# Kernel tuning notes

Hardware: AMD Instinct MI355X
Metric: run time of the kernel (lower is better)

Reference implementation:

```python
import jax, jax.numpy as jnp
import numpy as np

N_HEAD = 16
OUTPUT_DIM = 1024
HEAD_DIM = OUTPUT_DIM // N_HEAD  # 64


def setup_inputs() -> dict:
    key = jax.random.key(0)
    kq, kk, kv = jax.random.split(key, 3)
    B, S, D = 4, 2048, OUTPUT_DIM
    return {
        "Q": jax.random.normal(kq, (B, S, D), dtype=jnp.float32),
        "K": jax.random.normal(kk, (B, S, D), dtype=jnp.float32),
        "V": jax.random.normal(kv, (B, S, D), dtype=jnp.float32),
    }


def reference(Q, K, V):
    # FAITHFUL to the original Keras layer: it reshapes Q into K and V as well
    # (K = reshape(Q, ...), V = reshape(Q, ...)), so the K and V inputs are
    # ignored and attention is computed of Q against itself.
    B, S, _ = Q.shape
    q = Q.reshape(B, S, N_HEAD, HEAD_DIM)  # [B,S,H,D]
    scale = 1.0 / np.sqrt(HEAD_DIM).astype(np.float32)
    # scores: [B,H,S,S]
    scores = jnp.einsum("bshd,bthd->bhst", q, q) * scale
    attn = jax.nn.softmax(scores, axis=-1)
    out = jnp.einsum("bhst,bthd->bshd", attn, q)  # [B,S,H,D]
    # concat of per-head slices along last axis == head-major reshape
    return out.reshape(B, S, N_HEAD * HEAD_DIM)
```

## Files before the change

### kernel.cpp

```cpp
#include <hip/hip_runtime.h>
#include <stdint.h>

#define S_LEN 2048
#define DH    64
#define NH    16
#define DM    1024
#define NBH   64

typedef float    f32x4 __attribute__((ext_vector_type(4)));
typedef _Float16 half8 __attribute__((ext_vector_type(8)));
typedef _Float16 half4 __attribute__((ext_vector_type(4)));

#define GL_LDS_B128(g, l) \
  __builtin_amdgcn_global_load_lds((const __attribute__((address_space(1))) void*)(g), \
                                   (__attribute__((address_space(3))) void*)(l), 16, 0, 0)

__global__ __launch_bounds__(256) void preprocess_kernel(const float* __restrict__ Q,
                                                         _Float16* __restrict__ Qh,
                                                         _Float16* __restrict__ QhT) {
    const int t  = threadIdx.x;
    const int st = blockIdx.x & 31;
    const int bh = blockIdx.x >> 5;
    const int b = bh >> 4, h = bh & 15;
    const int s0 = (t & 15) * 4;
    const int d0 = (t >> 4) * 4;
    const float* src = Q + (size_t)b * S_LEN * DM + (size_t)(st * 64) * DM + h * DH;

    half4 hv[4];
    #pragma unroll
    for (int i = 0; i < 4; ++i) {
        const float4 v = *(const float4*)(src + (size_t)(s0 + i) * DM + d0);
        hv[i] = (half4){ (_Float16)v.x, (_Float16)v.y, (_Float16)v.z, (_Float16)v.w };
    }
    _Float16* qh = Qh + ((size_t)bh * S_LEN + st * 64) * DH;
    #pragma unroll
    for (int i = 0; i < 4; ++i)
        *(half4*)(qh + (s0 + i) * DH + d0) = hv[i];
    _Float16* qt = QhT + (size_t)bh * DH * S_LEN + st * 64;
    #pragma unroll
    for (int j = 0; j < 4; ++j) {
        const half4 tv = (half4){ hv[0][j], hv[1][j], hv[2][j], hv[3][j] };
        *(half4*)(qt + (size_t)(d0 + j) * S_LEN + s0) = tv;
    }
}

__global__ __launch_bounds__(128, 2) void attn_v3_kernel(const _Float16* __restrict__ Qh,
                                                         const _Float16* __restrict__ QhT,
                                                         float* __restrict__ out) {
    __shared__ __align__(16) _Float16 KnS[64 * 64];
    __shared__ __align__(16) _Float16 KtS[64 * 64];
    __shared__ __align__(16) _Float16 Pb[2][64 * 64];

    const int tid  = threadIdx.x;
    const int w    = tid >> 6;
    const int lane = tid & 63;
    const int quad = lane >> 4;
    const int l15  = lane & 15;
    const int xq   = l15 & 7;
    const int qblk = blockIdx.x & 15;
    const int bh   = blockIdx.x >> 4;
    const int q0   = qblk * 128 + w * 64;

    const _Float16* qh_bh = Qh + (size_t)bh * S_LEN * DH;
    const _Float16* qt_bh = QhT + (size_t)bh * DH * S_LEN;

    half8 qreg[4][2];
    #pragma unroll
    for (int nch = 0; nch < 4; ++nch) {
        const _Float16* p = qh_bh + (size_t)(q0 + nch * 16 + l15) * DH + quad * 8;
        qreg[nch][0] = *(const half8*)p;
        qreg[nch][1] = *(const half8*)(p + 32);
    }

    const float qs = 0.18033688011112042f;
    float m_c[4];
    #pragma unroll
    for (int nch = 0; nch < 4; ++nch) {
        float part = 0.f;
        #pragma unroll
        for (int s = 0; s < 2; ++s)
            #pragma unroll
            for (int j = 0; j < 8; ++j) { const float x = (float)qreg[nch][s][j]; part += x * x; }
        part += __shfl_xor(part, 16, 64);
        part += __shfl_xor(part, 32, 64);
        m_c[nch] = qs * part;
    }

    const _Float16* kn_src[4]; _Float16* kn_dst[4];
    const _Float16* kt_src[4]; _Float16* kt_dst[4];
    #pragma unroll
    for (int i = 0; i < 4; ++i) {
        const int ch = i * 128 + tid;
        const int row = ch >> 3, c = ch & 7;
        kn_src[i] = qh_bh + row * DH + ((c ^ (row & 7)) * 8);
        kn_dst[i] = &KnS[ch * 8];
        kt_src[i] = qt_bh + (size_t)row * S_LEN + ((c ^ (row & 7)) * 8);
        kt_dst[i] = &KtS[ch * 8];
    }

    f32x4 O[4][4];
    #pragma unroll
    for (int m = 0; m < 4; ++m)
        #pragma unroll
        for (int n = 0; n < 4; ++n) O[m][n] = (f32x4){0.f, 0.f, 0.f, 0.f};
    float lsum[4] = {0.f, 0.f, 0.f, 0.f};
    _Float16* Pw = Pb[w];

    for (int t = 0; t < S_LEN / 64; ++t) {
        __syncthreads();
        #pragma unroll
        for (int i = 0; i < 4; ++i) GL_LDS_B128(kn_src[i] + t * (64 * DH), kn_dst[i]);
        #pragma unroll
        for (int i = 0; i < 4; ++i) GL_LDS_B128(kt_src[i] + t * 64, kt_dst[i]);
        __syncthreads();

        #pragma unroll
        for (int mch = 0; mch < 4; ++mch) {
            const half8 a0 = *(const half8*)&KnS[(mch * 16 + l15) * 64 + ((quad ^ xq) * 8)];
            const half8 a1 = *(const half8*)&KnS[(mch * 16 + l15) * 64 + (((4 + quad) ^ xq) * 8)];
            const int wc   = 2 * mch + (quad >> 1);
            const int woff = (quad & 1) * 4;
            #pragma unroll
            for (int nch = 0; nch < 4; ++nch) {
                f32x4 acc = (f32x4){0.f, 0.f, 0.f, 0.f};
                acc = __builtin_amdgcn_mfma_f32_16x16x32_f16(a0, qreg[nch][0], acc, 0, 0, 0);
                acc = __builtin_amdgcn_mfma_f32_16x16x32_f16(a1, qreg[nch][1], acc, 0, 0, 0);
                const float p0 = __builtin_amdgcn_exp2f(__builtin_fmaf(acc[0], qs, -m_c[nch]));
                const float p1 = __builtin_amdgcn_exp2f(__builtin_fmaf(acc[1], qs, -m_c[nch]));
                const float p2 = __builtin_amdgcn_exp2f(__builtin_fmaf(acc[2], qs, -m_c[nch]));
                const float p3 = __builtin_amdgcn_exp2f(__builtin_fmaf(acc[3], qs, -m_c[nch]));
                lsum[nch] += (p0 + p1) + (p2 + p3);
                const half4 hv = (half4){ (_Float16)p0, (_Float16)p1, (_Float16)p2, (_Float16)p3 };
                *(half4*)&Pw[(nch * 16 + l15) * 64 + ((wc ^ xq) * 8) + woff] = hv;
            }
        }

        half8 pf[4][2];
        #pragma unroll
        for (int mch = 0; mch < 4; ++mch) {
            pf[mch][0] = *(const half8*)&Pw[(mch * 16 + l15) * 64 + ((quad ^ xq) * 8)];
            pf[mch][1] = *(const half8*)&Pw[(mch * 16 + l15) * 64 + (((4 + quad) ^ xq) * 8)];
        }
        #pragma unroll
        for (int nch = 0; nch < 4; ++nch) {
            const half8 v0 = *(const half8*)&KtS[(nch * 16 + l15) * 64 + ((quad ^ xq) * 8)];
            const half8 v1 = *(const half8*)&KtS[(nch * 16 + l15) * 64 + (((4 + quad) ^ xq) * 8)];
            #pragma unroll
            for (int mch = 0; mch < 4; ++mch) {
                O[mch][nch] = __builtin_amdgcn_mfma_f32_16x16x32_f16(pf[mch][0], v0, O[mch][nch], 0, 0, 0);
                O[mch][nch] = __builtin_amdgcn_mfma_f32_16x16x32_f16(pf[mch][1], v1, O[mch][nch], 0, 0, 0);
            }
        }
    }

    float lcol[4];
    #pragma unroll
    for (int nch = 0; nch < 4; ++nch) {
        float l = lsum[nch];
        l += __shfl_xor(l, 16, 64);
        l += __shfl_xor(l, 32, 64);
        lcol[nch] = l;
    }
    const int b = bh >> 4, h = bh & 15;
    float* ob = out + (size_t)b * S_LEN * DM + h * DH;
    #pragma unroll
    for (int mch = 0; mch < 4; ++mch) {
        float inv[4];
        #pragma unroll
        for (int r = 0; r < 4; ++r)
            inv[r] = 1.0f / __shfl(lcol[mch], quad * 4 + r, 16);
        #pragma unroll
        for (int nch = 0; nch < 4; ++nch)
            #pragma unroll
            for (int r = 0; r < 4; ++r)
                ob[(size_t)(q0 + mch * 16 + quad * 4 + r) * DM + nch * 16 + l15] = O[mch][nch][r] * inv[r];
    }
}

extern "C" void kernel_launch(void* const* d_in, const int* in_sizes, int n_in,
                              void* d_out, int out_size, void* d_ws, size_t ws_size,
                              hipStream_t stream) {
    const float* Q = (const float*)d_in[0];
    float* out = (float*)d_out;
    _Float16* Qh  = (_Float16*)d_ws;
    _Float16* QhT = Qh + (size_t)NBH * S_LEN * DH;
    preprocess_kernel<<<dim3(NBH * (S_LEN / 64)), dim3(256), 0, stream>>>(Q, Qh, QhT);
    attn_v3_kernel<<<dim3(NBH * (S_LEN / 128)), dim3(128), 0, stream>>>(Qh, QhT, out);
}
```

Baseline: 215.0 us.

## Split attention blocks into four 32-query waves and transpose via LDS in preprocess

The attention kernel now runs 256 threads per block, with four waves of 32 queries each instead of two waves of 64, and launch bounds allow more blocks per CU. Each wave holds half the accumulator and Q registers, which is meant to raise occupancy and latency hiding. In exchange, each K tile staged in LDS feeds fewer MFMAs per wave, so there is more LDS traffic and barrier overhead per unit of work. The preprocess kernel now stages a 64x64 tile in padded LDS so both the fp16 row-major and transposed outputs are written with coalesced 16-byte stores.

```diff
diff --git a/kernel.cpp b/kernel.cpp
--- a/kernel.cpp
+++ b/kernel.cpp
@@ -18,38 +18,57 @@
 __global__ __launch_bounds__(256) void preprocess_kernel(const float* __restrict__ Q,
                                                          _Float16* __restrict__ Qh,
                                                          _Float16* __restrict__ QhT) {
+    __shared__ __align__(16) _Float16 tile[64][72];
     const int t  = threadIdx.x;
     const int st = blockIdx.x & 31;
     const int bh = blockIdx.x >> 5;
     const int b = bh >> 4, h = bh & 15;
-    const int s0 = (t & 15) * 4;
-    const int d0 = (t >> 4) * 4;
-    const float* src = Q + (size_t)b * S_LEN * DM + (size_t)(st * 64) * DM + h * DH;
-
-    half4 hv[4];
-    #pragma unroll
-    for (int i = 0; i < 4; ++i) {
-        const float4 v = *(const float4*)(src + (size_t)(s0 + i) * DM + d0);
-        hv[i] = (half4){ (_Float16)v.x, (_Float16)v.y, (_Float16)v.z, (_Float16)v.w };
-    }
-    _Float16* qh = Qh + ((size_t)bh * S_LEN + st * 64) * DH;
-    #pragma unroll
-    for (int i = 0; i < 4; ++i)
-        *(half4*)(qh + (s0 + i) * DH + d0) = hv[i];
-    _Float16* qt = QhT + (size_t)bh * DH * S_LEN + st * 64;
-    #pragma unroll
-    for (int j = 0; j < 4; ++j) {
-        const half4 tv = (half4){ hv[0][j], hv[1][j], hv[2][j], hv[3][j] };
-        *(half4*)(qt + (size_t)(d0 + j) * S_LEN + s0) = tv;
+    const int s0 = st * 64;
+
+    {
+        const int r = t >> 2;
+        const int c = (t & 3) * 16;
+        const float* src = Q + ((size_t)b * S_LEN + s0 + r) * DM + h * DH + c;
+        #pragma unroll
+        for (int i = 0; i < 4; ++i) {
+            const float4 v = ((const float4*)src)[i];
+            *(half4*)&tile[r][c + 4 * i] =
+                (half4){ (_Float16)v.x, (_Float16)v.y, (_Float16)v.z, (_Float16)v.w };
+        }
+    }
+    __syncthreads();
+
+    {
+        const int s = t >> 2;
+        const int c = (t & 3) * 16;
+        const half8 a = *(const half8*)&tile[s][c];
+        const half8 b8 = *(const half8*)&tile[s][c + 8];
+        _Float16* dst = Qh + ((size_t)bh * S_LEN + s0 + s) * DH + c;
+        *(half8*)dst = a;
+        *(half8*)(dst + 8) = b8;
+    }
+
+    {
+        const int d  = t >> 2;
+        const int sg = (t & 3) * 16;
+        half8 x0, x1;
+        #pragma unroll
+        for (int j = 0; j < 8; ++j) {
+            x0[j] = tile[sg + j][d];
+            x1[j] = tile[sg + 8 + j][d];
+        }
+        _Float16* dst = QhT + ((size_t)bh * DH + d) * S_LEN + s0 + sg;
+        *(half8*)dst = x0;
+        *(half8*)(dst + 8) = x1;
     }
 }
 
-__global__ __launch_bounds__(128, 2) void attn_v3_kernel(const _Float16* __restrict__ Qh,
+__global__ __launch_bounds__(256, 4) void attn_v4_kernel(const _Float16* __restrict__ Qh,
                                                          const _Float16* __restrict__ QhT,
                                                          float* __restrict__ out) {
     __shared__ __align__(16) _Float16 KnS[64 * 64];
     __shared__ __align__(16) _Float16 KtS[64 * 64];
-    __shared__ __align__(16) _Float16 Pb[2][64 * 64];
+    __shared__ __align__(16) _Float16 Pb[4][32 * 64];
 
     const int tid  = threadIdx.x;
     const int w    = tid >> 6;
@@ -59,23 +78,23 @@
     const int xq   = l15 & 7;
     const int qblk = blockIdx.x & 15;
     const int bh   = blockIdx.x >> 4;
-    const int q0   = qblk * 128 + w * 64;
+    const int q0   = qblk * 128 + w * 32;
 
     const _Float16* qh_bh = Qh + (size_t)bh * S_LEN * DH;
     const _Float16* qt_bh = QhT + (size_t)bh * DH * S_LEN;
 
-    half8 qreg[4][2];
-    #pragma unroll
-    for (int nch = 0; nch < 4; ++nch) {
+    half8 qreg[2][2];
+    #pragma unroll
+    for (int nch = 0; nch < 2; ++nch) {
         const _Float16* p = qh_bh + (size_t)(q0 + nch * 16 + l15) * DH + quad * 8;
         qreg[nch][0] = *(const half8*)p;
         qreg[nch][1] = *(const half8*)(p + 32);
     }
 
     const float qs = 0.18033688011112042f;
-    float m_c[4];
-    #pragma unroll
-    for (int nch = 0; nch < 4; ++nch) {
+    float m_c[2];
+    #pragma unroll
+    for (int nch = 0; nch < 2; ++nch) {
         float part = 0.f;
         #pragma unroll
         for (int s = 0; s < 2; ++s)
@@ -86,11 +105,11 @@
         m_c[nch] = qs * part;
     }
 
-    const _Float16* kn_src[4]; _Float16* kn_dst[4];
-    const _Float16* kt_src[4]; _Float16* kt_dst[4];
-    #pragma unroll
-    for (int i = 0; i < 4; ++i) {
-        const int ch = i * 128 + tid;
+    const _Float16* kn_src[2]; _Float16* kn_dst[2];
+    const _Float16* kt_src[2]; _Float16* kt_dst[2];
+    #pragma unroll
+    for (int i = 0; i < 2; ++i) {
+        const int ch = i * 256 + tid;
         const int row = ch >> 3, c = ch & 7;
         kn_src[i] = qh_bh + row * DH + ((c ^ (row & 7)) * 8);
         kn_dst[i] = &KnS[ch * 8];
@@ -98,20 +117,20 @@
         kt_dst[i] = &KtS[ch * 8];
     }
 
-    f32x4 O[4][4];
-    #pragma unroll
-    for (int m = 0; m < 4; ++m)
+    f32x4 O[2][4];
+    #pragma unroll
+    for (int m = 0; m < 2; ++m)
         #pragma unroll
         for (int n = 0; n < 4; ++n) O[m][n] = (f32x4){0.f, 0.f, 0.f, 0.f};
-    float lsum[4] = {0.f, 0.f, 0.f, 0.f};
+    float lsum[2] = {0.f, 0.f};
     _Float16* Pw = Pb[w];
 
     for (int t = 0; t < S_LEN / 64; ++t) {
         __syncthreads();
         #pragma unroll
-        for (int i = 0; i < 4; ++i) GL_LDS_B128(kn_src[i] + t * (64 * DH), kn_dst[i]);
-        #pragma unroll
-        for (int i = 0; i < 4; ++i) GL_LDS_B128(kt_src[i] + t * 64, kt_dst[i]);
+        for (int i = 0; i < 2; ++i) GL_LDS_B128(kn_src[i] + t * (64 * DH), kn_dst[i]);
+        #pragma unroll
+        for (int i = 0; i < 2; ++i) GL_LDS_B128(kt_src[i] + t * 64, kt_dst[i]);
         __syncthreads();
 
         #pragma unroll
@@ -121,7 +140,7 @@
             const int wc   = 2 * mch + (quad >> 1);
             const int woff = (quad & 1) * 4;
             #pragma unroll
-            for (int nch = 0; nch < 4; ++nch) {
+            for (int nch = 0; nch < 2; ++nch) {
                 f32x4 acc = (f32x4){0.f, 0.f, 0.f, 0.f};
                 acc = __builtin_amdgcn_mfma_f32_16x16x32_f16(a0, qreg[nch][0], acc, 0, 0, 0);
                 acc = __builtin_amdgcn_mfma_f32_16x16x32_f16(a1, qreg[nch][1], acc, 0, 0, 0);
@@ -135,45 +154,45 @@
             }
         }
 
-        half8 pf[4][2];
-        #pragma unroll
-        for (int mch = 0; mch < 4; ++mch) {
-            pf[mch][0] = *(const half8*)&Pw[(mch * 16 + l15) * 64 + ((quad ^ xq) * 8)];
-            pf[mch][1] = *(const half8*)&Pw[(mch * 16 + l15) * 64 + (((4 + quad) ^ xq) * 8)];
+        half8 pf[2][2];
+        #pragma unroll
+        for (int qb = 0; qb < 2; ++qb) {
+            pf[qb][0] = *(const half8*)&Pw[(qb * 16 + l15) * 64 + ((quad ^ xq) * 8)];
+            pf[qb][1] = *(const half8*)&Pw[(qb * 16 + l15) * 64 + (((4 + quad) ^ xq) * 8)];
         }
         #pragma unroll
         for (int nch = 0; nch < 4; ++nch) {
             const half8 v0 = *(const half8*)&KtS[(nch * 16 + l15) * 64 + ((quad ^ xq) * 8)];
             const half8 v1 = *(const half8*)&KtS[(nch * 16 + l15) * 64 + (((4 + quad) ^ xq) * 8)];
             #pragma unroll
-            for (int mch = 0; mch < 4; ++mch) {
-                O[mch][nch] = __builtin_amdgcn_mfma_f32_16x16x32_f16(pf[mch][0], v0, O[mch][nch], 0, 0, 0);
-                O[mch][nch] = __builtin_amdgcn_mfma_f32_16x16x32_f16(pf[mch][1], v1, O[mch][nch], 0, 0, 0);
+            for (int qb = 0; qb < 2; ++qb) {
+                O[qb][nch] = __builtin_amdgcn_mfma_f32_16x16x32_f16(pf[qb][0], v0, O[qb][nch], 0, 0, 0);
+                O[qb][nch] = __builtin_amdgcn_mfma_f32_16x16x32_f16(pf[qb][1], v1, O[qb][nch], 0, 0, 0);
             }
         }
     }
 
-    float lcol[4];
-    #pragma unroll
-    for (int nch = 0; nch < 4; ++nch) {
-        float l = lsum[nch];
+    float lcol[2];
+    #pragma unroll
+    for (int qb = 0; qb < 2; ++qb) {
+        float l = lsum[qb];
         l += __shfl_xor(l, 16, 64);
         l += __shfl_xor(l, 32, 64);
-        lcol[nch] = l;
+        lcol[qb] = l;
     }
     const int b = bh >> 4, h = bh & 15;
     float* ob = out + (size_t)b * S_LEN * DM + h * DH;
     #pragma unroll
-    for (int mch = 0; mch < 4; ++mch) {
+    for (int qb = 0; qb < 2; ++qb) {
         float inv[4];
         #pragma unroll
         for (int r = 0; r < 4; ++r)
-            inv[r] = 1.0f / __shfl(lcol[mch], quad * 4 + r, 16);
+            inv[r] = 1.0f / __shfl(lcol[qb], quad * 4 + r, 16);
         #pragma unroll
         for (int nch = 0; nch < 4; ++nch)
             #pragma unroll
             for (int r = 0; r < 4; ++r)
-                ob[(size_t)(q0 + mch * 16 + quad * 4 + r) * DM + nch * 16 + l15] = O[mch][nch][r] * inv[r];
+                ob[(size_t)(q0 + qb * 16 + quad * 4 + r) * DM + nch * 16 + l15] = O[qb][nch][r] * inv[r];
     }
 }
 
@@ -185,5 +204,5 @@
     _Float16* Qh  = (_Float16*)d_ws;
     _Float16* QhT = Qh + (size_t)NBH * S_LEN * DH;
     preprocess_kernel<<<dim3(NBH * (S_LEN / 64)), dim3(256), 0, stream>>>(Q, Qh, QhT);
-    attn_v3_kernel<<<dim3(NBH * (S_LEN / 128)), dim3(128), 0, stream>>>(Qh, QhT, out);
+    attn_v4_kernel<<<dim3(NBH * (S_LEN / 128)), dim3(256), 0, stream>>>(Qh, QhT, out);
 }
```

After: 211.1 us. About the same (-1.8%).
